# Performance work log

Hardware: AMD Instinct MI355X
Metric: run time of the kernel (lower is better)

Reference implementation:

```python
import jax, jax.numpy as jnp
import numpy as np
import math

MAX_DELAY = 25
TAU = 2.0
VTH = 1.0
BN_EPS = 1e-5
ATAN_ALPHA = 2.0


def build_dcls_kernel(W, P, SIG, D):
    # Gaussian-interpolated DCLS kernel ('gauss' version).
    # W, P, SIG: (O, I, K) -> kernel (O, I, D)
    lim = D // 2
    j = jnp.arange(D, dtype=W.dtype)                      # (D,)
    Pc = jnp.clip(P, -lim, lim) + lim                     # (O, I, K)
    sig = jnp.abs(SIG) + 0.27
    g = jnp.exp(-0.5 * ((j - Pc[..., None]) / sig[..., None]) ** 2)  # (O,I,K,D)
    g = g / (g.sum(-1, keepdims=True) + 1e-7)
    return jnp.einsum('oik,oikd->oid', W, g)


def dcls_conv_positive(x, W, P, SIG, D):
    # Dale-positive: abs(weight) before kernel construction; padding=0 (VALID)
    k = build_dcls_kernel(jnp.abs(W), P, SIG, D)
    return jax.lax.conv_general_dilated(
        x, k, window_strides=(1,), padding='VALID',
        dimension_numbers=('NCW', 'OIW', 'NCW'))


def batchnorm_m(x, gamma, beta):
    # spikingjelly layer.BatchNorm1d step_mode='m' on (T, B, C):
    # flattens (T*B) as batch, normalizes per channel (training-mode stats).
    mean = x.mean(axis=(0, 1))
    var = x.var(axis=(0, 1))
    return (x - mean) * jax.lax.rsqrt(var + BN_EPS) * gamma + beta


def lif_multistep(x_seq, tau, v_th):
    # LIFNode, decay_input=False, v_reset=0 (hard reset), detach_reset=True,
    # ATan surrogate. x_seq: (T, B, C).
    inv_tau = jnp.asarray(1.0 / tau, x_seq.dtype)
    def step(v, xt):
        v = v * (1.0 - inv_tau) + xt              # charge (decay_input=False)
        u = v - v_th
        sg = jnp.arctan(0.5 * math.pi * ATAN_ALPHA * u) / math.pi + 0.5
        hard = (u >= 0).astype(xt.dtype)
        spike = sg + jax.lax.stop_gradient(hard - sg)
        v = v * (1.0 - jax.lax.stop_gradient(spike))   # hard reset, detached
        return v, spike
    v0 = jnp.zeros(x_seq.shape[1:], x_seq.dtype)
    _, spikes = jax.lax.scan(step, v0, x_seq)
    return spikes


def setup_inputs() -> dict:
    key = jax.random.key(0)
    ks = jax.random.split(key, 8)
    B, C_in, T = 64, 700, 300
    n_out, n_inh, K = 256, 128, 1
    return {
        'x': jax.random.normal(ks[0], (B, C_in, T), jnp.float32),
        'W_inh': jax.random.normal(ks[1], (n_inh, C_in, K), jnp.float32),
        'P_inh': jax.random.normal(ks[2], (n_inh, C_in, K), jnp.float32),
        'SIG_inh': jax.random.uniform(ks[3], (n_inh, C_in, K), jnp.float32),
        'W_exc': jax.random.normal(ks[4], (n_out, C_in, K), jnp.float32),
        'P_exc': jax.random.normal(ks[5], (n_out, C_in, K), jnp.float32),
        'SIG_exc': jax.random.uniform(ks[6], (n_out, C_in, K), jnp.float32),
        'w_exc_inh': jax.random.uniform(ks[7], (n_out, n_inh), jnp.float32),
        'bn_gamma': jnp.ones((n_inh,), jnp.float32),
        'bn_beta': jnp.zeros((n_inh,), jnp.float32),
    }


def reference(x, W_inh, P_inh, SIG_inh, W_exc, P_exc, SIG_exc, w_exc_inh,
              bn_gamma, bn_beta):
    # inhibitory branch
    in_inhib = dcls_conv_positive(x, W_inh, P_inh, SIG_inh, MAX_DELAY)  # (B,Ci,T')
    in_inhib = jnp.transpose(in_inhib, (2, 0, 1))                       # (T',B,Ci)
    in_inhib = batchnorm_m(in_inhib, bn_gamma, bn_beta)
    spikes = lif_multistep(in_inhib, TAU, VTH)                          # (T',B,Ci)
    out_inhib = jnp.einsum('tbi,oi->tbo', spikes, -jnp.abs(w_exc_inh))
    out_inhib = jnp.transpose(out_inhib, (1, 2, 0))                     # (B,O,T')
    # excitatory branch
    excit = dcls_conv_positive(x, W_exc, P_exc, SIG_exc, MAX_DELAY)     # (B,O,T')
    return excit + out_inhib
```

## Files before the change

kernel.cpp:

```cpp
#include <hip/hip_runtime.h>
#include <math.h>

#define CI   700
#define TIN  300
#define DD   25
#define TOUT 276
#define BB   64
#define OINH 128
#define OEXC 256

#define TROWS 312
#define IPAD  704

typedef __attribute__((ext_vector_type(8))) short short8;
typedef __attribute__((ext_vector_type(4))) float f32x4;
typedef __attribute__((ext_vector_type(8))) unsigned short ushort8v;

static __device__ __forceinline__ unsigned short f2bf(float f) {
    unsigned int u = __float_as_uint(f);
    unsigned int r = (u + 0x7FFFu + ((u >> 16) & 1u)) >> 16;
    return (unsigned short)r;
}
static __device__ __forceinline__ float bf2f(unsigned short h) {
    return __uint_as_float(((unsigned int)h) << 16);
}

static __device__ __forceinline__ void gload_lds16(const void* g, void* l) {
    __builtin_amdgcn_global_load_lds(
        (const __attribute__((address_space(1))) unsigned int*)g,
        (__attribute__((address_space(3))) unsigned int*)l, 16, 0, 0);
}

__global__ void build_kt(const float* __restrict__ W, const float* __restrict__ P,
                         const float* __restrict__ SIG, float* __restrict__ kt, int O) {
    int n = blockIdx.x * 256 + threadIdx.x;
    if (n >= O * CI) return;
    int o = n % O;
    int i = n / O;
    float w   = fabsf(W[o * CI + i]);
    float p   = fminf(fmaxf(P[o * CI + i], -12.f), 12.f) + 12.f;
    float sig = fabsf(SIG[o * CI + i]) + 0.27f;
    float inv = 1.f / sig;
    float g[DD];
    float sum = 0.f;
#pragma unroll
    for (int d = 0; d < DD; ++d) {
        float e = ((float)d - p) * inv;
        g[d] = expf(-0.5f * e * e);
        sum += g[d];
    }
    float sc = w / (sum + 1e-7f);
#pragma unroll
    for (int d = 0; d < DD; ++d)
        kt[(i * DD + d) * O + o] = g[d] * sc;
}

__global__ void kexc_build(const float* __restrict__ W, const float* __restrict__ P,
                           const float* __restrict__ SIG, unsigned short* __restrict__ kb2) {
    int n = blockIdx.x * 256 + threadIdx.x;
    if (n >= OEXC * IPAD) return;
    int o = n / IPAD, ip = n % IPAD;
    if (ip >= CI) {
#pragma unroll
        for (int d = 0; d < DD; ++d)
            kb2[((size_t)d * OEXC + o) * IPAD + ip] = 0;
        return;
    }
    float w   = fabsf(W[o * CI + ip]);
    float p   = fminf(fmaxf(P[o * CI + ip], -12.f), 12.f) + 12.f;
    float sig = fabsf(SIG[o * CI + ip]) + 0.27f;
    float inv = 1.f / sig;
    float g[DD];
    float sum = 0.f;
#pragma unroll
    for (int d = 0; d < DD; ++d) {
        float e = ((float)d - p) * inv;
        g[d] = expf(-0.5f * e * e);
        sum += g[d];
    }
    float sc = w / (sum + 1e-7f);
#pragma unroll
    for (int d = 0; d < DD; ++d)
        kb2[((size_t)d * OEXC + o) * IPAD + ip] = f2bf(g[d] * sc);
}

__global__ void kinh_build(const float* __restrict__ W, const float* __restrict__ P,
                           const float* __restrict__ SIG,
                           unsigned short* __restrict__ kbh, unsigned short* __restrict__ kbl) {
    int n = blockIdx.x * 256 + threadIdx.x;
    if (n >= OINH * IPAD) return;
    int o = n / IPAD, ip = n % IPAD;
    if (ip >= CI) {
#pragma unroll
        for (int d = 0; d < DD; ++d) {
            kbh[((size_t)d * OINH + o) * IPAD + ip] = 0;
            kbl[((size_t)d * OINH + o) * IPAD + ip] = 0;
        }
        return;
    }
    float w   = fabsf(W[o * CI + ip]);
    float p   = fminf(fmaxf(P[o * CI + ip], -12.f), 12.f) + 12.f;
    float sig = fabsf(SIG[o * CI + ip]) + 0.27f;
    float inv = 1.f / sig;
    float g[DD];
    float sum = 0.f;
#pragma unroll
    for (int d = 0; d < DD; ++d) {
        float e = ((float)d - p) * inv;
        g[d] = expf(-0.5f * e * e);
        sum += g[d];
    }
    float sc = w / (sum + 1e-7f);
#pragma unroll
    for (int d = 0; d < DD; ++d) {
        float v = g[d] * sc;
        unsigned short h = f2bf(v);
        kbh[((size_t)d * OINH + o) * IPAD + ip] = h;
        kbl[((size_t)d * OINH + o) * IPAD + ip] = f2bf(v - bf2f(h));
    }
}

__global__ __launch_bounds__(256)
void xt_kernel(const float* __restrict__ x, unsigned short* __restrict__ xTh,
               unsigned short* __restrict__ xTl) {
    __shared__ float tile[64][65];
    const int tid = threadIdx.x;
    const int t0 = blockIdx.x * 64, i0 = blockIdx.y * 64, b = blockIdx.z;
#pragma unroll
    for (int s = 0; s < 16; ++s) {
        int f = s * 256 + tid;
        int tt = f & 63, ii = f >> 6;
        float v = 0.f;
        if (t0 + tt < TIN && i0 + ii < CI)
            v = x[((size_t)b * CI + i0 + ii) * TIN + t0 + tt];
        tile[tt][ii] = v;
    }
    __syncthreads();
#pragma unroll
    for (int s = 0; s < 2; ++s) {
        int f = s * 256 + tid;
        int tt = f >> 3, g = f & 7;
        if (t0 + tt < TROWS) {
            ushort8v vh, vl;
#pragma unroll
            for (int e = 0; e < 8; ++e) {
                float v = tile[tt][g * 8 + e];
                unsigned short h = f2bf(v);
                vh[e] = h;
                vl[e] = f2bf(v - bf2f(h));
            }
            size_t off = ((size_t)b * TROWS + t0 + tt) * IPAD + i0 + g * 8;
            *(ushort8v*)(xTh + off) = vh;
            if (xTl) *(ushort8v*)(xTl + off) = vl;
        }
    }
}

__global__ void wt_kernel(const float* __restrict__ w, float* __restrict__ wt) {
    int n = blockIdx.x * 256 + threadIdx.x;
    if (n >= OINH * OEXC) return;
    int o = n % OEXC, c = n / OEXC;
    wt[c * OEXC + o] = -fabsf(w[o * OINH + c]);
}

__global__ __launch_bounds__(256, 3)
void conv_fused_v7(const unsigned short* __restrict__ xTh, const unsigned short* __restrict__ xTl,
                   const unsigned short* __restrict__ kb2,
                   const unsigned short* __restrict__ kbh, const unsigned short* __restrict__ kbl,
                   float* __restrict__ pexc0, float* __restrict__ pexc1,
                   float* __restrict__ pinh0, float* __restrict__ pinh1) {
    __shared__ unsigned short lds[24576];

    const int tid  = threadIdx.x;
    const int wave = tid >> 6;
    const int lane = tid & 63;
    const int wb   = wave >> 1;
    const int wo   = wave & 1;
    const int l15 = lane & 15, l4 = lane >> 4;
    const int tt   = blockIdx.x % 3;
    const int ksp  = blockIdx.x / 3;
    const int role = blockIdx.y;
    const int bp   = blockIdx.z;
    const int t0   = tt * 96;
    const int icb  = ksp * 11;

    const int ld_r = lane >> 2;
    const int ld_c = (((lane & 3) ^ ((lane >> 3) & 3)) << 4);
    const int SA   = (l15 >> 1) & 3;

    const size_t xstride = (size_t)IPAD * 2;

    if (role < 2) {
        const int o0  = role * 128;
        const int o0w = o0 + wo * 64;
        const int b   = 2 * bp + wb;

        f32x4 acc[4][6];
#pragma unroll
        for (int i = 0; i < 4; ++i)
#pragma unroll
            for (int j = 0; j < 6; ++j) acc[i][j] = (f32x4)0.f;

        for (int c = 0; c < 11; ++c) {
            const size_t cb = (size_t)(icb + c) * 64;
            __syncthreads();
            for (int j = wave; j < 16; j += 4) {
                const int q = j >> 3, jj = j & 7;
                const char* xb = (const char*)xTh +
                    ((size_t)(2 * bp + q) * TROWS + t0) * xstride;
                gload_lds16(xb + (size_t)(16 * jj + ld_r) * xstride + cb + ld_c,
                            (char*)lds + q * 8192 + jj * 1024);
            }
            {
                const char* kbase = (const char*)kb2 + (size_t)o0w * xstride + cb;
                char* kdst = (char*)lds + 16384 + (0 * 2 + wo) * 4096;
#pragma unroll
                for (int j = 0; j < 4; ++j)
                    gload_lds16(kbase + (size_t)(16 * j + ld_r) * xstride + ld_c,
                                kdst + j * 1024);
            }
            asm volatile("s_waitcnt vmcnt(0)" ::: "memory");
            __syncthreads();

            for (int d = 0; d < DD; ++d) {
                const int cur = d & 1;
                if (d < DD - 1) {
                    const char* kbase = (const char*)kb2 +
                        ((size_t)((d + 1) * OEXC) + o0w) * xstride + cb;
                    char* kdst = (char*)lds + 16384 + ((cur ^ 1) * 2 + wo) * 4096;
#pragma unroll
                    for (int j = 0; j < 4; ++j)
                        gload_lds16(kbase + (size_t)(16 * j + ld_r) * xstride + ld_c,
                                    kdst + j * 1024);
                }
                const char* kp = (const char*)lds + 16384 + (cur * 2 + wo) * 4096;
                short8 A[4];
#pragma unroll
                for (int i = 0; i < 4; ++i)
                    A[i] = *(const short8*)(kp + (i * 16 + l15) * 64 + ((l4 ^ SA) << 4));
#pragma unroll
                for (int j = 0; j < 6; ++j) {
                    const int tr = j * 16 + l15 + d;
                    short8 Bv = *(const short8*)((const char*)lds + wb * 8192 + tr * 64 +
                                                 ((l4 ^ ((tr >> 1) & 3)) << 4));
#pragma unroll
                    for (int i = 0; i < 4; ++i)
                        acc[i][j] = __builtin_amdgcn_mfma_f32_16x16x32_bf16(
                            A[i], Bv, acc[i][j], 0, 0, 0);
                }
                asm volatile("s_waitcnt vmcnt(0)" ::: "memory");
                __syncthreads();
            }
        }
        float* dst = ksp ? pexc1 : pexc0;
#pragma unroll
        for (int i = 0; i < 4; ++i)
#pragma unroll
            for (int j = 0; j < 6; ++j) {
                const int t = t0 + j * 16 + l15;
                if (t < TOUT) {
                    float* op = dst + ((size_t)b * OEXC + o0w + i * 16 + l4 * 4) * TOUT + t;
#pragma unroll
                    for (int r = 0; r < 4; ++r) op[(size_t)r * TOUT] = acc[i][j][r];
                }
            }
    } else {
        const int o0  = (role - 2) * 64;
        const int o0w = o0 + wo * 32;
        const int b   = 2 * bp + wb;

        f32x4 acc[2][6];
#pragma unroll
        for (int i = 0; i < 2; ++i)
#pragma unroll
            for (int j = 0; j < 6; ++j) acc[i][j] = (f32x4)0.f;

        for (int c = 0; c < 11; ++c) {
            const size_t cb = (size_t)(icb + c) * 64;
            __syncthreads();
            for (int j = wave; j < 16; j += 4) {
                const int q = j >> 3, jj = j & 7;
                const size_t rowoff = ((size_t)(2 * bp + q) * TROWS + t0) * xstride +
                                      (size_t)(16 * jj + ld_r) * xstride + cb + ld_c;
                gload_lds16((const char*)xTh + rowoff,
                            (char*)lds + q * 8192 + jj * 1024);
                gload_lds16((const char*)xTl + rowoff,
                            (char*)lds + 16384 + q * 8192 + jj * 1024);
            }
            {
                const size_t ko = (size_t)o0w * xstride + cb;
                char* kdst = (char*)lds + 32768 + (0 * 2 + wo) * 4096;
#pragma unroll
                for (int j = 0; j < 2; ++j) {
                    gload_lds16((const char*)kbh + ko + (size_t)(16 * j + ld_r) * xstride + ld_c,
                                kdst + j * 1024);
                    gload_lds16((const char*)kbl + ko + (size_t)(16 * j + ld_r) * xstride + ld_c,
                                kdst + 2048 + j * 1024);
                }
            }
            asm volatile("s_waitcnt vmcnt(0)" ::: "memory");
            __syncthreads();

            for (int d = 0; d < DD; ++d) {
                const int cur = d & 1;
                if (d < DD - 1) {
                    const size_t ko = ((size_t)((d + 1) * OINH) + o0w) * xstride + cb;
                    char* kdst = (char*)lds + 32768 + ((cur ^ 1) * 2 + wo) * 4096;
#pragma unroll
                    for (int j = 0; j < 2; ++j) {
                        gload_lds16((const char*)kbh + ko + (size_t)(16 * j + ld_r) * xstride + ld_c,
                                    kdst + j * 1024);
                        gload_lds16((const char*)kbl + ko + (size_t)(16 * j + ld_r) * xstride + ld_c,
                                    kdst + 2048 + j * 1024);
                    }
                }
                const char* kp = (const char*)lds + 32768 + (cur * 2 + wo) * 4096;
                short8 Ah[2], Al[2];
#pragma unroll
                for (int i = 0; i < 2; ++i) {
                    Ah[i] = *(const short8*)(kp + (i * 16 + l15) * 64 + ((l4 ^ SA) << 4));
                    Al[i] = *(const short8*)(kp + 2048 + (i * 16 + l15) * 64 + ((l4 ^ SA) << 4));
                }
#pragma unroll
                for (int j = 0; j < 6; ++j) {
                    const int tr = j * 16 + l15 + d;
                    const int xo = tr * 64 + ((l4 ^ ((tr >> 1) & 3)) << 4);
                    short8 Bh = *(const short8*)((const char*)lds + wb * 8192 + xo);
                    short8 Bl = *(const short8*)((const char*)lds + 16384 + wb * 8192 + xo);
#pragma unroll
                    for (int i = 0; i < 2; ++i) {
                        acc[i][j] = __builtin_amdgcn_mfma_f32_16x16x32_bf16(
                            Ah[i], Bh, acc[i][j], 0, 0, 0);
                        acc[i][j] = __builtin_amdgcn_mfma_f32_16x16x32_bf16(
                            Ah[i], Bl, acc[i][j], 0, 0, 0);
                        acc[i][j] = __builtin_amdgcn_mfma_f32_16x16x32_bf16(
                            Al[i], Bh, acc[i][j], 0, 0, 0);
                    }
                }
                asm volatile("s_waitcnt vmcnt(0)" ::: "memory");
                __syncthreads();
            }
        }
        float* dst = ksp ? pinh1 : pinh0;
#pragma unroll
        for (int i = 0; i < 2; ++i)
#pragma unroll
            for (int j = 0; j < 6; ++j) {
                const int t = t0 + j * 16 + l15;
                if (t < TOUT) {
                    float* op = dst + ((size_t)b * OINH + o0w + i * 16 + l4 * 4) * TOUT + t;
#pragma unroll
                    for (int r = 0; r < 4; ++r) op[(size_t)r * TOUT] = acc[i][j][r];
                }
            }
    }
}

__global__ void add_exc(const float* __restrict__ p1, float* __restrict__ out) {
    int n = blockIdx.x * 256 + threadIdx.x;
    float4 a = ((const float4*)out)[n];
    float4 v = ((const float4*)p1)[n];
    a.x += v.x; a.y += v.y; a.z += v.z; a.w += v.w;
    ((float4*)out)[n] = a;
}

__global__ void bn_stats2(float* __restrict__ cinh, const float* __restrict__ q1,
                          const float* __restrict__ gamma, const float* __restrict__ beta,
                          float* __restrict__ scale, float* __restrict__ shift) {
    const int c = blockIdx.x, tid = threadIdx.x;
    float sum = 0.f, sq = 0.f;
    for (int idx = tid; idx < BB * TOUT; idx += 256) {
        int b = idx / TOUT, t = idx - b * TOUT;
        size_t off = (size_t)(b * OINH + c) * TOUT + t;
        float v = cinh[off] + q1[off];
        cinh[off] = v;
        sum += v; sq += v * v;
    }
#pragma unroll
    for (int off = 32; off; off >>= 1) {
        sum += __shfl_down(sum, off);
        sq  += __shfl_down(sq, off);
    }
    __shared__ float ls[8];
    int wid = tid >> 6;
    if ((tid & 63) == 0) { ls[wid * 2] = sum; ls[wid * 2 + 1] = sq; }
    __syncthreads();
    if (tid == 0) {
        float S = 0.f, Q = 0.f;
#pragma unroll
        for (int wv = 0; wv < 4; ++wv) { S += ls[wv * 2]; Q += ls[wv * 2 + 1]; }
        const float n = (float)(BB * TOUT);
        float mean = S / n;
        float var  = Q / n - mean * mean;
        float rs   = 1.f / sqrtf(var + 1e-5f);
        float sc   = gamma[c] * rs;
        scale[c] = sc;
        shift[c] = beta[c] - mean * sc;
    }
}

__global__ __launch_bounds__(128)
void lif2(const float* __restrict__ cinh, const float* __restrict__ scale,
          const float* __restrict__ shift, unsigned char* __restrict__ spk) {
    __shared__ float tile[128 * 65];
    const int b = blockIdx.x, c = threadIdx.x;
    const float sc = scale[c], sh = shift[c];
    const float* base = cinh + (size_t)b * OINH * TOUT;
    float v = 0.f;
    for (int tc = 0; tc < TOUT; tc += 64) {
        const int len = (TOUT - tc < 64) ? (TOUT - tc) : 64;
        const int L4 = len >> 2;
        __syncthreads();
        for (int q = c; q < 128 * L4; q += 128) {
            int cc = q / L4, e = q - cc * L4;
            float4 vv = *(const float4*)(base + (size_t)cc * TOUT + tc + e * 4);
            float* dstp = &tile[cc * 65 + e * 4];
            dstp[0] = vv.x; dstp[1] = vv.y; dstp[2] = vv.z; dstp[3] = vv.w;
        }
        __syncthreads();
        for (int t2 = 0; t2 < len; ++t2) {
            float xin = tile[c * 65 + t2] * sc + sh;
            v = 0.5f * v + xin;
            bool s = (v >= 1.f);
            spk[((size_t)(tc + t2) * BB + b) * OINH + c] = s ? 1 : 0;
            v = s ? 0.f : v;
        }
    }
}

__global__ __launch_bounds__(128)
void conv_mfma(const unsigned short* __restrict__ xTh, const unsigned short* __restrict__ kb2,
               float* __restrict__ out) {
    __shared__ unsigned short xs[120 * 64];
    __shared__ unsigned short ks[2][2][64 * 64];

    const int tid  = threadIdx.x;
    const int wave = tid >> 6;
    const int lane = tid & 63;
    const int l15 = lane & 15, l4 = lane >> 4, l7 = lane & 7;
    const int b  = blockIdx.z;
    const int t0 = blockIdx.x * 96;
    const int o0 = blockIdx.y * 128 + wave * 64;

    const int ld_row = lane >> 3;
    const int ld_swz = ((l7 ^ ld_row) << 4);

    f32x4 acc[4][6];
#pragma unroll
    for (int i = 0; i < 4; ++i)
#pragma unroll
        for (int j = 0; j < 6; ++j) acc[i][j] = (f32x4)0.f;

    const char* xrow0 = (const char*)xTh + ((size_t)b * TROWS + t0) * (IPAD * 2);

    for (int ic = 0; ic < 11; ++ic) {
        const int ic0 = ic * 64;
        __syncthreads();
        for (int j = wave; j < 15; j += 2)
            gload_lds16(xrow0 + (size_t)(8 * j + ld_row) * (IPAD * 2) + ic0 * 2 + ld_swz,
                        (char*)xs + j * 1024);
        {
            const char* ksrc = (const char*)kb2 + ((size_t)o0) * (IPAD * 2) + ic0 * 2;
            char* kdst = (char*)ks + (0 * 2 + wave) * 8192;
#pragma unroll
            for (int j = 0; j < 8; ++j)
                gload_lds16(ksrc + (size_t)(8 * j + ld_row) * (IPAD * 2) + ld_swz,
                            kdst + j * 1024);
        }
        asm volatile("s_waitcnt vmcnt(0)" ::: "memory");
        __syncthreads();

        for (int d = 0; d < DD; ++d) {
            const int cur = d & 1;
            if (d < DD - 1) {
                const char* ksrc = (const char*)kb2 +
                    ((size_t)(d + 1) * OEXC + o0) * (IPAD * 2) + ic0 * 2;
                char* kdst = (char*)ks + ((cur ^ 1) * 2 + wave) * 8192;
#pragma unroll
                for (int j = 0; j < 8; ++j)
                    gload_lds16(ksrc + (size_t)(8 * j + ld_row) * (IPAD * 2) + ld_swz,
                                kdst + j * 1024);
            }
            const char* kp = (const char*)ks + (cur * 2 + wave) * 8192;
#pragma unroll
            for (int ks2 = 0; ks2 < 2; ++ks2) {
                const int cg = ks2 * 4 + l4;
                short8 A[4];
#pragma unroll
                for (int i = 0; i < 4; ++i)
                    A[i] = *(const short8*)(kp + (i * 16 + l15) * 128 + ((cg ^ l7) << 4));
#pragma unroll
                for (int j = 0; j < 6; ++j) {
                    const int tr = j * 16 + l15 + d;
                    short8 Bv = *(const short8*)((const char*)xs + tr * 128 +
                                                 ((cg ^ (tr & 7)) << 4));
#pragma unroll
                    for (int i = 0; i < 4; ++i)
                        acc[i][j] = __builtin_amdgcn_mfma_f32_16x16x32_bf16(
                            A[i], Bv, acc[i][j], 0, 0, 0);
                }
            }
            asm volatile("s_waitcnt vmcnt(0)" ::: "memory");
        }
    }

#pragma unroll
    for (int i = 0; i < 4; ++i)
#pragma unroll
        for (int j = 0; j < 6; ++j) {
            const int tt = t0 + j * 16 + l15;
            if (tt < TOUT) {
                float* op = out + ((size_t)b * OEXC + o0 + i * 16 + l4 * 4) * TOUT + tt;
#pragma unroll
                for (int r = 0; r < 4; ++r) op[(size_t)r * TOUT] = acc[i][j][r];
            }
        }
}

__global__ __launch_bounds__(128)
void conv_mfma_inh(const unsigned short* __restrict__ xTh, const unsigned short* __restrict__ xTl,
                   const unsigned short* __restrict__ kbh, const unsigned short* __restrict__ kbl,
                   float* __restrict__ cinh) {
    __shared__ unsigned short xsh[120 * 64];
    __shared__ unsigned short xsl[120 * 64];
    __shared__ unsigned short ksh[2][64 * 64];
    __shared__ unsigned short ksl[2][64 * 64];

    const int tid  = threadIdx.x;
    const int wave = tid >> 6;
    const int lane = tid & 63;
    const int l15 = lane & 15, l4 = lane >> 4, l7 = lane & 7;
    const int b  = blockIdx.z;
    const int t0 = blockIdx.x * 96;
    const int o0 = blockIdx.y * 64;
    const int wtb = wave * 48;

    const int ld_row = lane >> 3;
    const int ld_swz = ((l7 ^ ld_row) << 4);

    f32x4 acc[4][3];
#pragma unroll
    for (int i = 0; i < 4; ++i)
#pragma unroll
        for (int j = 0; j < 3; ++j) acc[i][j] = (f32x4)0.f;

    const char* xrh = (const char*)xTh + ((size_t)b * TROWS + t0) * (IPAD * 2);
    const char* xrl = (const char*)xTl + ((size_t)b * TROWS + t0) * (IPAD * 2);
    const unsigned short* kb = wave ? kbl : kbh;

    for (int ic = 0; ic < 11; ++ic) {
        const int ic0 = ic * 64;
        __syncthreads();
        for (int j = wave; j < 15; j += 2) {
            gload_lds16(xrh + (size_t)(8 * j + ld_row) * (IPAD * 2) + ic0 * 2 + ld_swz,
                        (char*)xsh + j * 1024);
            gload_lds16(xrl + (size_t)(8 * j + ld_row) * (IPAD * 2) + ic0 * 2 + ld_swz,
                        (char*)xsl + j * 1024);
        }
        {
            char* kd = wave ? (char*)ksl[0] : (char*)ksh[0];
#pragma unroll
            for (int j = 0; j < 8; ++j)
                gload_lds16((const char*)kb +
                                ((size_t)(0 * OINH + o0 + 8 * j + ld_row)) * (IPAD * 2) +
                                ic0 * 2 + ld_swz,
                            kd + j * 1024);
        }
        asm volatile("s_waitcnt vmcnt(0)" ::: "memory");
        __syncthreads();

        for (int d = 0; d < DD; ++d) {
            const int cur = d & 1;
            if (d < DD - 1) {
                char* kd = wave ? (char*)ksl[cur ^ 1] : (char*)ksh[cur ^ 1];
#pragma unroll
                for (int j = 0; j < 8; ++j)
                    gload_lds16((const char*)kb +
                                    ((size_t)((d + 1) * OINH + o0 + 8 * j + ld_row)) * (IPAD * 2) +
                                    ic0 * 2 + ld_swz,
                                kd + j * 1024);
            }
            const char* kph = (const char*)ksh[cur];
            const char* kpl = (const char*)ksl[cur];
#pragma unroll
            for (int k2 = 0; k2 < 2; ++k2) {
                const int cg = k2 * 4 + l4;
                short8 Ah[4], Al[4];
#pragma unroll
                for (int i = 0; i < 4; ++i) {
                    Ah[i] = *(const short8*)(kph + (i * 16 + l15) * 128 + ((cg ^ l7) << 4));
                    Al[i] = *(const short8*)(kpl + (i * 16 + l15) * 128 + ((cg ^ l7) << 4));
                }
#pragma unroll
                for (int j = 0; j < 3; ++j) {
                    const int tr = wtb + j * 16 + l15 + d;
                    short8 Bh = *(const short8*)((const char*)xsh + tr * 128 +
                                                 ((cg ^ (tr & 7)) << 4));
                    short8 Bl = *(const short8*)((const char*)xsl + tr * 128 +
                                                 ((cg ^ (tr & 7)) << 4));
#pragma unroll
                    for (int i = 0; i < 4; ++i) {
                        acc[i][j] = __builtin_amdgcn_mfma_f32_16x16x32_bf16(
                            Ah[i], Bh, acc[i][j], 0, 0, 0);
                        acc[i][j] = __builtin_amdgcn_mfma_f32_16x16x32_bf16(
                            Ah[i], Bl, acc[i][j], 0, 0, 0);
                        acc[i][j] = __builtin_amdgcn_mfma_f32_16x16x32_bf16(
                            Al[i], Bh, acc[i][j], 0, 0, 0);
                    }
                }
            }
            asm volatile("s_waitcnt vmcnt(0)" ::: "memory");
            __syncthreads();
        }
    }

#pragma unroll
    for (int i = 0; i < 4; ++i)
#pragma unroll
        for (int j = 0; j < 3; ++j) {
            const int tt = t0 + wtb + j * 16 + l15;
            if (tt < TOUT) {
                float* op = cinh + ((size_t)b * OINH + o0 + i * 16 + l4 * 4) * TOUT + tt;
#pragma unroll
                for (int r = 0; r < 4; ++r) op[(size_t)r * TOUT] = acc[i][j][r];
            }
        }
}

__global__ __launch_bounds__(256)
void conv_dcls_fb(const float* __restrict__ x, const float* __restrict__ kt,
                  float* __restrict__ out, int O) {
    __shared__ float k_lds[100 * 128];
    __shared__ float x_lds[4 * 88];

    const int tid = threadIdx.x;
    const int tx = tid & 7;
    const int ty = tid >> 3;
    const int b  = blockIdx.z;
    const int t0 = blockIdx.x * 64;
    const int o0 = blockIdx.y * 128;
    const int tlim = TIN - t0;

    float acc[4][8];
#pragma unroll
    for (int ro = 0; ro < 4; ++ro)
#pragma unroll
        for (int rt = 0; rt < 8; ++rt) acc[ro][rt] = 0.f;

    for (int chunk = 0; chunk < 175; ++chunk) {
        const int i0 = chunk * 4;
        __syncthreads();
#pragma unroll
        for (int s = 0; s < 13; ++s) {
            int f = tid + s * 256;
            if (f < 3200) {
                int j = f >> 5, o4 = f & 31;
                ((float4*)k_lds)[f] =
                    *(const float4*)(kt + (size_t)(i0 * DD + j) * O + o0 + o4 * 4);
            }
        }
        if (tid < 88) {
            int icc = tid / 22, wq = tid % 22;
            float4 v = make_float4(0.f, 0.f, 0.f, 0.f);
            if (wq * 4 < tlim)
                v = *(const float4*)(x + (size_t)(b * CI + i0 + icc) * TIN + t0 + wq * 4);
            ((float4*)x_lds)[tid] = v;
        }
        __syncthreads();
#pragma unroll
        for (int icc = 0; icc < 4; ++icc) {
            float xv[32];
#pragma unroll
            for (int wq = 0; wq < 8; ++wq)
                *(float4*)(xv + 4 * wq) = ((const float4*)(x_lds + icc * 88))[tx * 2 + wq];
#pragma unroll
            for (int d = 0; d < DD; ++d) {
                float4 kv = ((const float4*)(k_lds + (icc * DD + d) * 128))[ty];
                float kvv[4] = {kv.x, kv.y, kv.z, kv.w};
#pragma unroll
                for (int ro = 0; ro < 4; ++ro)
#pragma unroll
                    for (int rt = 0; rt < 8; ++rt)
                        acc[ro][rt] += kvv[ro] * xv[rt + d];
            }
        }
    }
    const int tvalid = TOUT - t0;
#pragma unroll
    for (int ro = 0; ro < 4; ++ro) {
        float* op = out + (size_t)(b * O + o0 + ty * 4 + ro) * TOUT + t0;
#pragma unroll
        for (int u = 0; u < 2; ++u) {
            int toff = tx * 8 + u * 4;
            if (toff < tvalid) {
                float4 v = make_float4(acc[ro][u * 4 + 0], acc[ro][u * 4 + 1],
                                       acc[ro][u * 4 + 2], acc[ro][u * 4 + 3]);
                *(float4*)(op + toff) = v;
            }
        }
    }
}

__global__ void bn_stats(const float* __restrict__ cinh, const float* __restrict__ gamma,
                         const float* __restrict__ beta, float* __restrict__ scale,
                         float* __restrict__ shift) {
    const int c = blockIdx.x, tid = threadIdx.x;
    float sum = 0.f, sq = 0.f;
    for (int idx = tid; idx < BB * TOUT; idx += 256) {
        int b = idx / TOUT, t = idx - b * TOUT;
        float v = cinh[(size_t)(b * OINH + c) * TOUT + t];
        sum += v; sq += v * v;
    }
#pragma unroll
    for (int off = 32; off; off >>= 1) {
        sum += __shfl_down(sum, off);
        sq  += __shfl_down(sq, off);
    }
    __shared__ float ls[8];
    int wid = tid >> 6;
    if ((tid & 63) == 0) { ls[wid * 2] = sum; ls[wid * 2 + 1] = sq; }
    __syncthreads();
    if (tid == 0) {
        float S = 0.f, Q = 0.f;
#pragma unroll
        for (int wv = 0; wv < 4; ++wv) { S += ls[wv * 2]; Q += ls[wv * 2 + 1]; }
        const float n = (float)(BB * TOUT);
        float mean = S / n;
        float var  = Q / n - mean * mean;
        float rs   = 1.f / sqrtf(var + 1e-5f);
        float sc   = gamma[c] * rs;
        scale[c] = sc;
        shift[c] = beta[c] - mean * sc;
    }
}

__global__ void lif_kernel(const float* __restrict__ cinh, const float* __restrict__ scale,
                           const float* __restrict__ shift, unsigned char* __restrict__ spk) {
    const int b = blockIdx.x, c = threadIdx.x;
    const float sc = scale[c], sh = shift[c];
    const float* row = cinh + (size_t)(b * OINH + c) * TOUT;
    float v = 0.f;
    for (int t = 0; t < TOUT; ++t) {
        float xin = row[t] * sc + sh;
        v = 0.5f * v + xin;
        unsigned char s = (v >= 1.f) ? 1 : 0;
        spk[((size_t)t * BB + b) * OINH + c] = s;
        v = (v >= 1.f) ? 0.f : v;
    }
}

__global__ __launch_bounds__(256)
void finale(const unsigned char* __restrict__ spk, const float* __restrict__ wt,
            float* __restrict__ out) {
    __shared__ float s_lds[64 * 129];
    const int tid = threadIdx.x;
    const int tx = tid & 15, ty = tid >> 4;
    const int b = blockIdx.z, t0 = blockIdx.x * 64, o0 = blockIdx.y * 64;

#pragma unroll
    for (int s = 0; s < 32; ++s) {
        int f = tid + s * 256;
        int tt = f >> 7, c = f & 127;
        float v = 0.f;
        if (t0 + tt < TOUT) v = (float)spk[((size_t)(t0 + tt) * BB + b) * OINH + c];
        s_lds[tt * 129 + c] = v;
    }
    __syncthreads();

    float acc[4][4] = {{0.f}};
#pragma unroll 4
    for (int c = 0; c < 128; ++c) {
        float4 wv = *(const float4*)(wt + c * OEXC + o0 + ty * 4);
        float wvv[4] = {wv.x, wv.y, wv.z, wv.w};
        float sv[4];
#pragma unroll
        for (int rt = 0; rt < 4; ++rt) sv[rt] = s_lds[(tx * 4 + rt) * 129 + c];
#pragma unroll
        for (int ro = 0; ro < 4; ++ro)
#pragma unroll
            for (int rt = 0; rt < 4; ++rt)
                acc[ro][rt] += wvv[ro] * sv[rt];
    }

    const int tvalid = TOUT - t0;
    if (tx * 4 < tvalid) {
#pragma unroll
        for (int ro = 0; ro < 4; ++ro) {
            float* op = out + (size_t)(b * OEXC + o0 + ty * 4 + ro) * TOUT + t0 + tx * 4;
            float4 v = *(float4*)op;
            v.x += acc[ro][0]; v.y += acc[ro][1]; v.z += acc[ro][2]; v.w += acc[ro][3];
            *(float4*)op = v;
        }
    }
}

extern "C" void kernel_launch(void* const* d_in, const int* in_sizes, int n_in,
                              void* d_out, int out_size, void* d_ws, size_t ws_size,
                              hipStream_t stream) {
    const float* x       = (const float*)d_in[0];
    const float* W_inh   = (const float*)d_in[1];
    const float* P_inh   = (const float*)d_in[2];
    const float* SIG_inh = (const float*)d_in[3];
    const float* W_exc   = (const float*)d_in[4];
    const float* P_exc   = (const float*)d_in[5];
    const float* SIG_exc = (const float*)d_in[6];
    const float* w_ei    = (const float*)d_in[7];
    const float* gamma   = (const float*)d_in[8];
    const float* beta    = (const float*)d_in[9];
    float* out = (float*)d_out;

    const size_t XT_ELEMS   = (size_t)BB * TROWS * IPAD;
    const size_t KEXC_ELEMS = (size_t)DD * OEXC * IPAD;
    const size_t KINH_ELEMS = (size_t)DD * OINH * IPAD;
    const size_t CINH_ELEMS = (size_t)BB * OINH * TOUT;
    const size_t PEXC_ELEMS = (size_t)BB * OEXC * TOUT;

    const size_t NEED_FAST = 2 * XT_ELEMS * 2 + KEXC_ELEMS * 2 + 2 * KINH_ELEMS * 2 +
                             CINH_ELEMS * 4 + OINH * OEXC * 4 + CINH_ELEMS;
    const size_t NEED_FAST2 = (2 * XT_ELEMS + KEXC_ELEMS + 2 * KINH_ELEMS) * 2 +
                              (PEXC_ELEMS + 2 * CINH_ELEMS + OINH * OEXC + 256) * 4 +
                              CINH_ELEMS;

    if (ws_size >= NEED_FAST2) {
        unsigned short* xTh = (unsigned short*)d_ws;
        unsigned short* xTl = xTh + XT_ELEMS;
        unsigned short* kb2 = xTl + XT_ELEMS;
        unsigned short* kbh = kb2 + KEXC_ELEMS;
        unsigned short* kbl = kbh + KINH_ELEMS;
        float* pexc1 = (float*)(kbl + KINH_ELEMS);
        float* cinh  = pexc1 + PEXC_ELEMS;
        float* pinh1 = cinh + CINH_ELEMS;
        float* wt    = pinh1 + CINH_ELEMS;
        float* scale = wt + OINH * OEXC;
        float* shift = scale + OINH;
        unsigned char* spk = (unsigned char*)(shift + OINH);

        hipLaunchKernelGGL(kexc_build, dim3((OEXC * IPAD + 255) / 256), dim3(256), 0, stream,
                           W_exc, P_exc, SIG_exc, kb2);
        hipLaunchKernelGGL(kinh_build, dim3((OINH * IPAD + 255) / 256), dim3(256), 0, stream,
                           W_inh, P_inh, SIG_inh, kbh, kbl);
        hipLaunchKernelGGL(xt_kernel, dim3(5, 11, 64), dim3(256), 0, stream, x, xTh, xTl);
        hipLaunchKernelGGL(wt_kernel, dim3(128), dim3(256), 0, stream, w_ei, wt);

        hipLaunchKernelGGL(conv_fused_v7, dim3(6, 4, 32), dim3(256), 0, stream,
                           xTh, xTl, kb2, kbh, kbl, out, pexc1, cinh, pinh1);

        hipLaunchKernelGGL(add_exc, dim3((unsigned)(PEXC_ELEMS / 4 / 256)), dim3(256), 0, stream,
                           pexc1, out);
        hipLaunchKernelGGL(bn_stats2, dim3(128), dim3(256), 0, stream,
                           cinh, pinh1, gamma, beta, scale, shift);
        hipLaunchKernelGGL(lif2, dim3(64), dim3(128), 0, stream, cinh, scale, shift, spk);
        hipLaunchKernelGGL(finale, dim3(5, 4, 64), dim3(256), 0, stream, spk, wt, out);
    } else if (ws_size >= NEED_FAST) {
        unsigned short* xTh = (unsigned short*)d_ws;
        unsigned short* xTl = xTh + XT_ELEMS;
        unsigned short* kb2 = xTl + XT_ELEMS;
        unsigned short* kbh = kb2 + KEXC_ELEMS;
        unsigned short* kbl = kbh + KINH_ELEMS;
        float* cinh  = (float*)(kbl + KINH_ELEMS);
        float* wt    = cinh + CINH_ELEMS;
        float* scale = wt + OINH * OEXC;
        float* shift = scale + OINH;
        unsigned char* spk = (unsigned char*)(shift + OINH);

        hipLaunchKernelGGL(kexc_build, dim3((OEXC * IPAD + 255) / 256), dim3(256), 0, stream,
                           W_exc, P_exc, SIG_exc, kb2);
        hipLaunchKernelGGL(kinh_build, dim3((OINH * IPAD + 255) / 256), dim3(256), 0, stream,
                           W_inh, P_inh, SIG_inh, kbh, kbl);
        hipLaunchKernelGGL(xt_kernel, dim3(5, 11, 64), dim3(256), 0, stream, x, xTh, xTl);
        hipLaunchKernelGGL(wt_kernel, dim3(128), dim3(256), 0, stream, w_ei, wt);

        hipLaunchKernelGGL(conv_mfma, dim3(3, 2, 64), dim3(128), 0, stream, xTh, kb2, out);
        hipLaunchKernelGGL(conv_mfma_inh, dim3(3, 2, 64), dim3(128), 0, stream,
                           xTh, xTl, kbh, kbl, cinh);

        hipLaunchKernelGGL(bn_stats, dim3(128), dim3(256), 0, stream, cinh, gamma, beta, scale, shift);
        hipLaunchKernelGGL(lif_kernel, dim3(64), dim3(128), 0, stream, cinh, scale, shift, spk);
        hipLaunchKernelGGL(finale, dim3(5, 4, 64), dim3(256), 0, stream, spk, wt, out);
    } else {
        unsigned short* xTh = (unsigned short*)d_ws;
        unsigned short* kb2 = xTh + XT_ELEMS;
        float* kt_inh = (float*)(kb2 + KEXC_ELEMS);
        float* cinh   = kt_inh + 2240000;
        float* wt     = cinh + CINH_ELEMS;
        float* scale  = wt + OINH * OEXC;
        float* shift  = scale + OINH;
        unsigned char* spk = (unsigned char*)(shift + OINH);

        hipLaunchKernelGGL(kexc_build, dim3((OEXC * IPAD + 255) / 256), dim3(256), 0, stream,
                           W_exc, P_exc, SIG_exc, kb2);
        hipLaunchKernelGGL(build_kt, dim3(350), dim3(256), 0, stream,
                           W_inh, P_inh, SIG_inh, kt_inh, OINH);
        hipLaunchKernelGGL(xt_kernel, dim3(5, 11, 64), dim3(256), 0, stream, x, xTh,
                           (unsigned short*)nullptr);
        hipLaunchKernelGGL(wt_kernel, dim3(128), dim3(256), 0, stream, w_ei, wt);

        hipLaunchKernelGGL(conv_mfma, dim3(3, 2, 64), dim3(128), 0, stream, xTh, kb2, out);
        hipLaunchKernelGGL(conv_dcls_fb, dim3(5, 1, 64), dim3(256), 0, stream, x, kt_inh, cinh, OINH);

        hipLaunchKernelGGL(bn_stats, dim3(128), dim3(256), 0, stream, cinh, gamma, beta, scale, shift);
        hipLaunchKernelGGL(lif_kernel, dim3(64), dim3(128), 0, stream, cinh, scale, shift, spk);
        hipLaunchKernelGGL(finale, dim3(5, 4, 64), dim3(256), 0, stream, spk, wt, out);
    }
}
```

Baseline: 479.0 us.

## Stage two delay taps per barrier in fused conv kernel

```diff
diff --git a/kernel.cpp b/kernel.cpp
--- a/kernel.cpp
+++ b/kernel.cpp
@@ -24,7 +24,6 @@
 static __device__ __forceinline__ float bf2f(unsigned short h) {
     return __uint_as_float(((unsigned int)h) << 16);
 }
-
 static __device__ __forceinline__ void gload_lds16(const void* g, void* l) {
     __builtin_amdgcn_global_load_lds(
         (const __attribute__((address_space(1))) unsigned int*)g,
@@ -35,19 +34,16 @@
                          const float* __restrict__ SIG, float* __restrict__ kt, int O) {
     int n = blockIdx.x * 256 + threadIdx.x;
     if (n >= O * CI) return;
-    int o = n % O;
-    int i = n / O;
+    int o = n % O, i = n / O;
     float w   = fabsf(W[o * CI + i]);
     float p   = fminf(fmaxf(P[o * CI + i], -12.f), 12.f) + 12.f;
     float sig = fabsf(SIG[o * CI + i]) + 0.27f;
     float inv = 1.f / sig;
-    float g[DD];
-    float sum = 0.f;
+    float g[DD]; float sum = 0.f;
 #pragma unroll
     for (int d = 0; d < DD; ++d) {
         float e = ((float)d - p) * inv;
-        g[d] = expf(-0.5f * e * e);
-        sum += g[d];
+        g[d] = expf(-0.5f * e * e); sum += g[d];
     }
     float sc = w / (sum + 1e-7f);
 #pragma unroll
@@ -70,13 +66,11 @@
     float p   = fminf(fmaxf(P[o * CI + ip], -12.f), 12.f) + 12.f;
     float sig = fabsf(SIG[o * CI + ip]) + 0.27f;
     float inv = 1.f / sig;
-    float g[DD];
-    float sum = 0.f;
+    float g[DD]; float sum = 0.f;
 #pragma unroll
     for (int d = 0; d < DD; ++d) {
         float e = ((float)d - p) * inv;
-        g[d] = expf(-0.5f * e * e);
-        sum += g[d];
+        g[d] = expf(-0.5f * e * e); sum += g[d];
     }
     float sc = w / (sum + 1e-7f);
 #pragma unroll
@@ -102,13 +96,11 @@
     float p   = fminf(fmaxf(P[o * CI + ip], -12.f), 12.f) + 12.f;
     float sig = fabsf(SIG[o * CI + ip]) + 0.27f;
     float inv = 1.f / sig;
-    float g[DD];
-    float sum = 0.f;
+    float g[DD]; float sum = 0.f;
 #pragma unroll
     for (int d = 0; d < DD; ++d) {
         float e = ((float)d - p) * inv;
-        g[d] = expf(-0.5f * e * e);
-        sum += g[d];
+        g[d] = expf(-0.5f * e * e); sum += g[d];
     }
     float sc = w / (sum + 1e-7f);
 #pragma unroll
@@ -163,13 +155,13 @@
     wt[c * OEXC + o] = -fabsf(w[o * OINH + c]);
 }
 
-__global__ __launch_bounds__(256, 3)
-void conv_fused_v7(const unsigned short* __restrict__ xTh, const unsigned short* __restrict__ xTl,
+__global__ __launch_bounds__(256, 2)
+void conv_fused_v8(const unsigned short* __restrict__ xTh, const unsigned short* __restrict__ xTl,
                    const unsigned short* __restrict__ kb2,
                    const unsigned short* __restrict__ kbh, const unsigned short* __restrict__ kbl,
                    float* __restrict__ pexc0, float* __restrict__ pexc1,
                    float* __restrict__ pinh0, float* __restrict__ pinh1) {
-    __shared__ unsigned short lds[24576];
+    __shared__ unsigned short lds[32768];
 
     const int tid  = threadIdx.x;
     const int wave = tid >> 6;
@@ -189,11 +181,10 @@
     const int SA   = (l15 >> 1) & 3;
 
     const size_t xstride = (size_t)IPAD * 2;
-
-    if (role < 2) {
-        const int o0  = role * 128;
-        const int o0w = o0 + wo * 64;
-        const int b   = 2 * bp + wb;
+    const int b = 2 * bp + wb;
+
+    if (role >= 2) {
+        const int o0w = (role - 2) * 128 + wo * 64;
 
         f32x4 acc[4][6];
 #pragma unroll
@@ -211,9 +202,11 @@
                 gload_lds16(xb + (size_t)(16 * jj + ld_r) * xstride + cb + ld_c,
                             (char*)lds + q * 8192 + jj * 1024);
             }
-            {
-                const char* kbase = (const char*)kb2 + (size_t)o0w * xstride + cb;
-                char* kdst = (char*)lds + 16384 + (0 * 2 + wo) * 4096;
+#pragma unroll
+            for (int s = 0; s < 2; ++s) {
+                const char* kbase = (const char*)kb2 +
+                    ((size_t)(s * OEXC) + o0w) * xstride + cb;
+                char* kdst = (char*)lds + 16384 + wo * 8192 + s * 4096;
 #pragma unroll
                 for (int j = 0; j < 4; ++j)
                     gload_lds16(kbase + (size_t)(16 * j + ld_r) * xstride + ld_c,
@@ -222,31 +215,44 @@
             asm volatile("s_waitcnt vmcnt(0)" ::: "memory");
             __syncthreads();
 
-            for (int d = 0; d < DD; ++d) {
-                const int cur = d & 1;
-                if (d < DD - 1) {
-                    const char* kbase = (const char*)kb2 +
-                        ((size_t)((d + 1) * OEXC) + o0w) * xstride + cb;
-                    char* kdst = (char*)lds + 16384 + ((cur ^ 1) * 2 + wo) * 4096;
-#pragma unroll
-                    for (int j = 0; j < 4; ++j)
-                        gload_lds16(kbase + (size_t)(16 * j + ld_r) * xstride + ld_c,
-                                    kdst + j * 1024);
+            for (int it = 0; it <= 12; ++it) {
+                const int d0 = 2 * it;
+                const int nb = (it + 1) & 1;
+#pragma unroll
+                for (int s = 0; s < 2; ++s) {
+                    const int dn = d0 + 2 + s;
+                    if (dn < DD) {
+                        const char* kbase = (const char*)kb2 +
+                            ((size_t)(dn * OEXC) + o0w) * xstride + cb;
+                        char* kdst = (char*)lds + 16384 + (nb * 2 + wo) * 8192 + s * 4096;
+#pragma unroll
+                        for (int j = 0; j < 4; ++j)
+                            gload_lds16(kbase + (size_t)(16 * j + ld_r) * xstride + ld_c,
+                                        kdst + j * 1024);
+                    }
                 }
-                const char* kp = (const char*)lds + 16384 + (cur * 2 + wo) * 4096;
-                short8 A[4];
-#pragma unroll
-                for (int i = 0; i < 4; ++i)
-                    A[i] = *(const short8*)(kp + (i * 16 + l15) * 64 + ((l4 ^ SA) << 4));
-#pragma unroll
-                for (int j = 0; j < 6; ++j) {
-                    const int tr = j * 16 + l15 + d;
-                    short8 Bv = *(const short8*)((const char*)lds + wb * 8192 + tr * 64 +
-                                                 ((l4 ^ ((tr >> 1) & 3)) << 4));
-#pragma unroll
-                    for (int i = 0; i < 4; ++i)
-                        acc[i][j] = __builtin_amdgcn_mfma_f32_16x16x32_bf16(
-                            A[i], Bv, acc[i][j], 0, 0, 0);
+#pragma unroll
+                for (int s = 0; s < 2; ++s) {
+                    const int d = d0 + s;
+                    if (d < DD) {
+                        const char* kp = (const char*)lds + 16384 +
+                                         ((it & 1) * 2 + wo) * 8192 + s * 4096;
+                        short8 A[4];
+#pragma unroll
+                        for (int i = 0; i < 4; ++i)
+                            A[i] = *(const short8*)(kp + (i * 16 + l15) * 64 +
+                                                    ((l4 ^ SA) << 4));
+#pragma unroll
+                        for (int j = 0; j < 6; ++j) {
+                            const int tr = j * 16 + l15 + d;
+                            short8 Bv = *(const short8*)((const char*)lds + wb * 8192 +
+                                                         tr * 64 + ((l4 ^ ((tr >> 1) & 3)) << 4));
+#pragma unroll
+                            for (int i = 0; i < 4; ++i)
+                                acc[i][j] = __builtin_amdgcn_mfma_f32_16x16x32_bf16(
+                                    A[i], Bv, acc[i][j], 0, 0, 0);
+                        }
+                    }
                 }
                 asm volatile("s_waitcnt vmcnt(0)" ::: "memory");
                 __syncthreads();
@@ -265,9 +271,7 @@
                 }
             }
     } else {
-        const int o0  = (role - 2) * 64;
-        const int o0w = o0 + wo * 32;
-        const int b   = 2 * bp + wb;
+        const int o0w = role * 64 + wo * 32;
 
         f32x4 acc[2][6];
 #pragma unroll
@@ -282,14 +286,13 @@
                 const int q = j >> 3, jj = j & 7;
                 const size_t rowoff = ((size_t)(2 * bp + q) * TROWS + t0) * xstride +
                                       (size_t)(16 * jj + ld_r) * xstride + cb + ld_c;
-                gload_lds16((const char*)xTh + rowoff,
-                            (char*)lds + q * 8192 + jj * 1024);
-                gload_lds16((const char*)xTl + rowoff,
-                            (char*)lds + 16384 + q * 8192 + jj * 1024);
-            }
-            {
-                const size_t ko = (size_t)o0w * xstride + cb;
-                char* kdst = (char*)lds + 32768 + (0 * 2 + wo) * 4096;
+                gload_lds16((const char*)xTh + rowoff, (char*)lds + q * 8192 + jj * 1024);
+                gload_lds16((const char*)xTl + rowoff, (char*)lds + 16384 + q * 8192 + jj * 1024);
+            }
+#pragma unroll
+            for (int s = 0; s < 2; ++s) {
+                const size_t ko = ((size_t)(s * OINH) + o0w) * xstride + cb;
+                char* kdst = (char*)lds + 32768 + wo * 8192 + s * 4096;
 #pragma unroll
                 for (int j = 0; j < 2; ++j) {
                     gload_lds16((const char*)kbh + ko + (size_t)(16 * j + ld_r) * xstride + ld_c,
@@ -301,40 +304,56 @@
             asm volatile("s_waitcnt vmcnt(0)" ::: "memory");
             __syncthreads();
 
-            for (int d = 0; d < DD; ++d) {
-                const int cur = d & 1;
-                if (d < DD - 1) {
-                    const size_t ko = ((size_t)((d + 1) * OINH) + o0w) * xstride + cb;
-                    char* kdst = (char*)lds + 32768 + ((cur ^ 1) * 2 + wo) * 4096;
-#pragma unroll
-                    for (int j = 0; j < 2; ++j) {
-                        gload_lds16((const char*)kbh + ko + (size_t)(16 * j + ld_r) * xstride + ld_c,
-                                    kdst + j * 1024);
-                        gload_lds16((const char*)kbl + ko + (size_t)(16 * j + ld_r) * xstride + ld_c,
-                                    kdst + 2048 + j * 1024);
+            for (int it = 0; it <= 12; ++it) {
+                const int d0 = 2 * it;
+                const int nb = (it + 1) & 1;
+#pragma unroll
+                for (int s = 0; s < 2; ++s) {
+                    const int dn = d0 + 2 + s;
+                    if (dn < DD) {
+                        const size_t ko = ((size_t)(dn * OINH) + o0w) * xstride + cb;
+                        char* kdst = (char*)lds + 32768 + (nb * 2 + wo) * 8192 + s * 4096;
+#pragma unroll
+                        for (int j = 0; j < 2; ++j) {
+                            gload_lds16((const char*)kbh + ko +
+                                            (size_t)(16 * j + ld_r) * xstride + ld_c,
+                                        kdst + j * 1024);
+                            gload_lds16((const char*)kbl + ko +
+                                            (size_t)(16 * j + ld_r) * xstride + ld_c,
+                                        kdst + 2048 + j * 1024);
+                        }
                     }
                 }
-                const char* kp = (const char*)lds + 32768 + (cur * 2 + wo) * 4096;
-                short8 Ah[2], Al[2];
-#pragma unroll
-                for (int i = 0; i < 2; ++i) {
-                    Ah[i] = *(const short8*)(kp + (i * 16 + l15) * 64 + ((l4 ^ SA) << 4));
-                    Al[i] = *(const short8*)(kp + 2048 + (i * 16 + l15) * 64 + ((l4 ^ SA) << 4));
-                }
-#pragma unroll
-                for (int j = 0; j < 6; ++j) {
-                    const int tr = j * 16 + l15 + d;
-                    const int xo = tr * 64 + ((l4 ^ ((tr >> 1) & 3)) << 4);
-                    short8 Bh = *(const short8*)((const char*)lds + wb * 8192 + xo);
-                    short8 Bl = *(const short8*)((const char*)lds + 16384 + wb * 8192 + xo);
-#pragma unroll
-                    for (int i = 0; i < 2; ++i) {
-                        acc[i][j] = __builtin_amdgcn_mfma_f32_16x16x32_bf16(
-                            Ah[i], Bh, acc[i][j], 0, 0, 0);
-                        acc[i][j] = __builtin_amdgcn_mfma_f32_16x16x32_bf16(
-                            Ah[i], Bl, acc[i][j], 0, 0, 0);
-                        acc[i][j] = __builtin_amdgcn_mfma_f32_16x16x32_bf16(
-                            Al[i], Bh, acc[i][j], 0, 0, 0);
+#pragma unroll
+                for (int s = 0; s < 2; ++s) {
+                    const int d = d0 + s;
+                    if (d < DD) {
+                        const char* kp = (const char*)lds + 32768 +
+                                         ((it & 1) * 2 + wo) * 8192 + s * 4096;
+                        short8 Ah[2], Al[2];
+#pragma unroll
+                        for (int i = 0; i < 2; ++i) {
+                            Ah[i] = *(const short8*)(kp + (i * 16 + l15) * 64 +
+                                                     ((l4 ^ SA) << 4));
+                            Al[i] = *(const short8*)(kp + 2048 + (i * 16 + l15) * 64 +
+                                                     ((l4 ^ SA) << 4));
+                        }
+#pragma unroll
+                        for (int j = 0; j < 6; ++j) {
+                            const int tr = j * 16 + l15 + d;
+                            const int xo = tr * 64 + ((l4 ^ ((tr >> 1) & 3)) << 4);
+                            short8 Bh = *(const short8*)((const char*)lds + wb * 8192 + xo);
+                            short8 Bl = *(const short8*)((const char*)lds + 16384 + wb * 8192 + xo);
+#pragma unroll
+                            for (int i = 0; i < 2; ++i) {
+                                acc[i][j] = __builtin_amdgcn_mfma_f32_16x16x32_bf16(
+                                    Ah[i], Bh, acc[i][j], 0, 0, 0);
+                                acc[i][j] = __builtin_amdgcn_mfma_f32_16x16x32_bf16(
+                                    Ah[i], Bl, acc[i][j], 0, 0, 0);
+                                acc[i][j] = __builtin_amdgcn_mfma_f32_16x16x32_bf16(
+                                    Al[i], Bh, acc[i][j], 0, 0, 0);
+                            }
+                        }
                     }
                 }
                 asm volatile("s_waitcnt vmcnt(0)" ::: "memory");
@@ -842,7 +861,7 @@
         hipLaunchKernelGGL(xt_kernel, dim3(5, 11, 64), dim3(256), 0, stream, x, xTh, xTl);
         hipLaunchKernelGGL(wt_kernel, dim3(128), dim3(256), 0, stream, w_ei, wt);
 
-        hipLaunchKernelGGL(conv_fused_v7, dim3(6, 4, 32), dim3(256), 0, stream,
+        hipLaunchKernelGGL(conv_fused_v8, dim3(6, 4, 32), dim3(256), 0, stream,
                            xTh, xTl, kb2, kbh, kbl, out, pexc1, cinh, pinh1);
 
         hipLaunchKernelGGL(add_exc, dim3((unsigned)(PEXC_ELEMS / 4 / 256)), dim3(256), 0, stream,
```

Result: slower. 495.2 us (+3.4%).
